# Optimization experiments

Hardware: AMD Instinct MI355X
Metric: run time of the kernel (lower is better)

## Reference

```python
import jax, jax.numpy as jnp
import numpy as np

D = 256      # input_dim
H = 8        # n_heads
HD = D // H  # head_dim = 32
S = 255      # num variables
S1 = S + 1   # new_seq (CLS + vars)
B = 4


def setup_inputs() -> dict:
    key = jax.random.key(0)
    ks = jax.random.split(key, 16)
    g = lambda k, shp, s=0.05: (jax.random.normal(k, shp, dtype=jnp.float32) * s)
    inp = {
        'desc_embeddings': jax.random.normal(ks[0], (B, S, D), dtype=jnp.float32),
        'name_value_embeddings': jax.random.normal(ks[1], (B, S1, D), dtype=jnp.float32),
        # q/k/v projections (nn.Linear: y = x @ W.T + b)
        'qW': g(ks[2], (D, D)), 'qb': jnp.zeros((D,), jnp.float32),
        'kW': g(ks[3], (D, D)), 'kb': jnp.zeros((D,), jnp.float32),
        'vW': g(ks[4], (D, D)), 'vb': jnp.zeros((D,), jnp.float32),
        # edge_update MLP: Linear(2D->D), LayerNorm(D), ReLU, Linear(D->D)
        'eW1': g(ks[5], (D, 2 * D)), 'eb1': jnp.zeros((D,), jnp.float32),
        'ln_g': jnp.ones((D,), jnp.float32), 'ln_b': jnp.zeros((D,), jnp.float32),
        'eW2': g(ks[6], (D, D)), 'eb2': jnp.zeros((D,), jnp.float32),
        # attn_proj: Linear(3*head_dim -> 1)
        'aW': g(ks[7], (1, 3 * HD)), 'ab': jnp.zeros((1,), jnp.float32),
    }
    return inp


def reference(desc_embeddings, name_value_embeddings, qW, qb, kW, kb, vW, vb,
              eW1, eb1, ln_g, ln_b, eW2, eb2, aW, ab):
    nve, desc = name_value_embeddings, desc_embeddings
    b, s1, _ = nve.shape
    s = s1 - 1

    # structure mask: CLS->Var on, Var->CLS off, Var-Var fully connected (self loops kept)
    new_adj = jnp.zeros((b, s1, s1), jnp.float32)
    new_adj = new_adj.at[:, 1:, 1:].set(1.0)
    new_adj = new_adj.at[:, 0, 1:].set(1.0)

    def lin(x, W, bb):
        return x @ W.T + bb

    q = lin(nve, qW, qb).reshape(b, s1, H, HD).transpose(0, 2, 1, 3)  # [B,H,S1,HD]
    k = lin(nve, kW, kb).reshape(b, s1, H, HD).transpose(0, 2, 1, 3)
    v = lin(nve, vW, vb).reshape(b, s1, H, HD).transpose(0, 2, 1, 3)

    # pairwise edge attributes [B,S1,S1,2D]
    di = jnp.broadcast_to(desc[:, :, None, :], (b, s, s, D))
    dj = jnp.broadcast_to(desc[:, None, :, :], (b, s, s, D))
    var_edge = jnp.concatenate([di, dj], axis=-1)              # [B,S,S,2D]
    cls_edge = jnp.concatenate([desc, desc], axis=-1)          # [B,S,2D]
    ea = jnp.zeros((b, s1, s1, 2 * D), jnp.float32)
    ea = ea.at[:, 1:, 1:].set(var_edge)
    ea = ea.at[:, 0, 1:].set(cls_edge)
    ea = ea.at[:, 1:, 0].set(cls_edge)

    # edge_update MLP (edge_type == 'mlp')
    h = lin(ea, eW1, eb1)
    mu = jnp.mean(h, axis=-1, keepdims=True)
    var = jnp.var(h, axis=-1, keepdims=True)
    h = ln_g * (h - mu) / jnp.sqrt(var + 1e-5) + ln_b
    h = jax.nn.relu(h)
    e = lin(h, eW2, eb2)                                       # [B,S1,S1,D]
    e = e.reshape(b, s1, s1, H, HD).transpose(0, 3, 1, 2, 4)    # [B,H,S1,S1,HD]
    e = e * new_adj[:, None, :, :, None]

    # attn_proj(cat(q_i, k_j, e_ij)) == q_i.wq + k_j.wk + e_ij.we + bias (gat_v1, no nonlinearity)
    wq, wk, we = aW[0, :HD], aW[0, HD:2 * HD], aW[0, 2 * HD:]
    logits = (jnp.einsum('bhid,d->bhi', q, wq)[:, :, :, None]
              + jnp.einsum('bhjd,d->bhj', k, wk)[:, :, None, :]
              + jnp.einsum('bhijd,d->bhij', e, we) + ab[0])    # [B,H,S1,S1]

    logits = logits + (new_adj[:, None] == 0).astype(logits.dtype) * -1e9
    attn = jax.nn.softmax(logits, axis=-1)                      # dropout omitted (eval)
    ctx = jnp.einsum('bhij,bhjd->bhid', attn, v)
    basis_outputs = ctx.transpose(0, 2, 1, 3)                   # [B,S1,H,HD]
    return basis_outputs, attn
```

## Files before the change

kernel.cpp:

```cpp
#include <hip/hip_runtime.h>
#include <math.h>

#define S 255
#define B 4

typedef _Float16 half8 __attribute__((ext_vector_type(8)));
typedef float f32x4 __attribute__((ext_vector_type(4)));

#define WS_APJ   0
#define WS_BPJ   131072
#define WS_VTF   262144
#define WS_ATT   393216
#define WS_AP    1441792
#define WS_GJ    1703936
#define WS_MFG   1966080
#define WS_CONST 1968128
#define WS_QLOG  1968192
#define WS_KLOG  1976384
#define WS_SA    1984576
#define WS_QA    1985600
#define WS_SB    1986624
#define WS_QB    1987648

__global__ __launch_bounds__(256) void k1(
    const float* __restrict__ desc, const float* __restrict__ nve,
    const float* __restrict__ qW, const float* __restrict__ qb,
    const float* __restrict__ kW, const float* __restrict__ kb,
    const float* __restrict__ vW, const float* __restrict__ vb,
    const float* __restrict__ eW1, const float* __restrict__ eb1,
    const float* __restrict__ eW2, const float* __restrict__ eb2,
    const float* __restrict__ aW, float* __restrict__ ws)
{
    const int blk = blockIdx.x;
    const int tid = threadIdx.x;
    __shared__ _Float16 Af[4096];
    __shared__ _Float16 Bf[4096];
    const int wave = tid >> 6, lane = tid & 63;
    const int m16 = lane & 15, quad = lane >> 4;
    const int sr = tid & 63, sko = (tid >> 6) * 16;
    const half8 z8 = {(_Float16)0,(_Float16)0,(_Float16)0,(_Float16)0,
                      (_Float16)0,(_Float16)0,(_Float16)0,(_Float16)0};

    if (blk < 192) {
        const float *X, *W; int M, wst, wof, jobt, sub = blk;
        if (sub < 64)       { X=nve;  W=vW;  M=1024; wst=256; wof=0;   jobt=0; }
        else if (sub < 128) { X=desc; W=eW1; M=1020; wst=512; wof=0;   jobt=1; sub-=64; }
        else                { X=desc; W=eW1; M=1020; wst=512; wof=256; jobt=2; sub-=128; }
        int mBase = (sub>>2)*64, nBase = (sub&3)*64;
        f32x4 acc[2][2] = {};
        for (int k0 = 0; k0 < 256; k0 += 64) {
            half8 xa[2], wb[2];
            int xr = mBase + sr, wr = nBase + sr;
            #pragma unroll
            for (int hh = 0; hh < 2; hh++) {
                int kk = k0 + sko + hh*8;
                if (xr < M) {
                    float4 x0 = *(const float4*)&X[xr*256 + kk];
                    float4 x1 = *(const float4*)&X[xr*256 + kk + 4];
                    half8 hv;
                    hv[0]=(_Float16)x0.x; hv[1]=(_Float16)x0.y; hv[2]=(_Float16)x0.z; hv[3]=(_Float16)x0.w;
                    hv[4]=(_Float16)x1.x; hv[5]=(_Float16)x1.y; hv[6]=(_Float16)x1.z; hv[7]=(_Float16)x1.w;
                    xa[hh] = hv;
                } else xa[hh] = z8;
                float4 w0 = *(const float4*)&W[wr*wst + wof + kk];
                float4 w1 = *(const float4*)&W[wr*wst + wof + kk + 4];
                half8 hw;
                hw[0]=(_Float16)w0.x; hw[1]=(_Float16)w0.y; hw[2]=(_Float16)w0.z; hw[3]=(_Float16)w0.w;
                hw[4]=(_Float16)w1.x; hw[5]=(_Float16)w1.y; hw[6]=(_Float16)w1.z; hw[7]=(_Float16)w1.w;
                wb[hh] = hw;
            }
            __syncthreads();
            #pragma unroll
            for (int hh = 0; hh < 2; hh++) {
                int krel = sko + hh*8;
                int c = krel >> 5, q2 = (krel >> 3) & 3;
                int ld = (sr & 15) + 16*q2, rt = sr >> 4;
                *(half8*)&Af[((rt*2 + c)*64 + ld)*8] = xa[hh];
                *(half8*)&Bf[((rt*2 + c)*64 + ld)*8] = wb[hh];
            }
            __syncthreads();
            int rt0 = (wave >> 1)*2, ct0 = (wave & 1)*2;
            #pragma unroll
            for (int c = 0; c < 2; c++) {
                half8 A0 = *(const half8*)&Af[(((rt0    )*2 + c)*64 + lane)*8];
                half8 A1 = *(const half8*)&Af[(((rt0 + 1)*2 + c)*64 + lane)*8];
                half8 B0 = *(const half8*)&Bf[(((ct0    )*2 + c)*64 + lane)*8];
                half8 B1 = *(const half8*)&Bf[(((ct0 + 1)*2 + c)*64 + lane)*8];
                acc[0][0] = __builtin_amdgcn_mfma_f32_16x16x32_f16(A0, B0, acc[0][0], 0,0,0);
                acc[0][1] = __builtin_amdgcn_mfma_f32_16x16x32_f16(A0, B1, acc[0][1], 0,0,0);
                acc[1][0] = __builtin_amdgcn_mfma_f32_16x16x32_f16(A1, B0, acc[1][0], 0,0,0);
                acc[1][1] = __builtin_amdgcn_mfma_f32_16x16x32_f16(A1, B1, acc[1][1], 0,0,0);
            }
        }
        int rt0 = (wave >> 1)*2, ct0 = (wave & 1)*2;
        if (jobt == 0) {
            _Float16* vtf = (_Float16*)(ws + WS_VTF);
            #pragma unroll
            for (int ci = 0; ci < 2; ci++) {
                int col = nBase + (ct0 + ci)*16 + m16;
                float bv = vb[col];
                int ct = col >> 4, n = col & 15;
                #pragma unroll
                for (int ri = 0; ri < 2; ri++)
                    #pragma unroll
                    for (int r = 0; r < 4; r++) {
                        int rr = mBase + (rt0 + ri)*16 + quad*4 + r;
                        int bb = rr >> 8, j = rr & 255;
                        int js = j >> 5, qv = (j >> 3) & 3, ev = j & 7;
                        float o = acc[ri][ci][r] + bv;
                        vtf[bb*65536 + (((ct*8 + js)*64 + n + 16*qv) << 3) + ev] = (_Float16)o;
                    }
            }
        } else {
            _Float16* OJ = (_Float16*)(ws + ((jobt == 1) ? WS_APJ : WS_BPJ));
            float* Sp = ws + ((jobt == 1) ? WS_SA : WS_SB);
            float* Qp = ws + ((jobt == 1) ? WS_QA : WS_QB);
            float svr[2][4] = {}, qvr[2][4] = {};
            #pragma unroll
            for (int ci = 0; ci < 2; ci++) {
                int col = nBase + (ct0 + ci)*16 + m16;
                float bv = (jobt == 1) ? eb1[col] : 0.f;
                int ks = col >> 5, q = (col >> 3) & 3, e = col & 7;
                #pragma unroll
                for (int ri = 0; ri < 2; ri++)
                    #pragma unroll
                    for (int r = 0; r < 4; r++) {
                        int rr = mBase + (rt0 + ri)*16 + quad*4 + r;
                        if (rr < 1020) {
                            float o = acc[ri][ci][r] + bv;
                            int bb = rr / 255;
                            int j = rr - bb*255 + 1;
                            int jt = j >> 4, mm = j & 15;
                            OJ[bb*65536 + (((jt*8 + ks)*64 + mm + 16*q) << 3) + e] = (_Float16)o;
                            if (jobt == 1) ws[WS_AP + rr*256 + col] = o;
                            svr[ri][r] += o;
                            qvr[ri][r] = fmaf(o, o, qvr[ri][r]);
                        }
                    }
            }
            #pragma unroll
            for (int ri = 0; ri < 2; ri++)
                #pragma unroll
                for (int r = 0; r < 4; r++) {
                    float s = svr[ri][r], q = qvr[ri][r];
                    #pragma unroll
                    for (int d = 1; d < 16; d <<= 1) {
                        s += __shfl_xor(s, d, 64);
                        q += __shfl_xor(q, d, 64);
                    }
                    int rr = mBase + (rt0 + ri)*16 + quad*4 + r;
                    if (m16 == 0 && rr < 1020) {
                        int bb = rr / 255;
                        int j = rr - bb*255 + 1;
                        atomicAdd(&Sp[bb*256 + j], s);
                        atomicAdd(&Qp[bb*256 + j], q);
                    }
                }
        }
    } else if (blk < 208) {
        {
            int d = tid;
            float f[16] = {0,0,0,0,0,0,0,0,0,0,0,0,0,0,0,0};
            for (int hd = 0; hd < 32; hd++) {
                float wq = aW[hd], wk = aW[32+hd];
                #pragma unroll
                for (int h = 0; h < 8; h++) {
                    f[h]   = fmaf(wq, qW[(h*32+hd)*256 + d], f[h]);
                    f[8+h] = fmaf(wk, kW[(h*32+hd)*256 + d], f[8+h]);
                }
            }
            int ksd = d >> 5, q2 = (d >> 3) & 3, jj = d & 7;
            #pragma unroll
            for (int n = 0; n < 16; n++)
                Bf[((ksd*64 + n + 16*q2))*8 + jj] = (_Float16)f[n];
        }
        __syncthreads();
        int mBase = (blk - 192)*64;
        f32x4 acc = {0.f,0.f,0.f,0.f};
        for (int k0 = 0; k0 < 256; k0 += 64) {
            half8 xa[2];
            #pragma unroll
            for (int hh = 0; hh < 2; hh++) {
                int kk = k0 + sko + hh*8;
                float4 x0 = *(const float4*)&nve[(mBase + sr)*256 + kk];
                float4 x1 = *(const float4*)&nve[(mBase + sr)*256 + kk + 4];
                half8 hv;
                hv[0]=(_Float16)x0.x; hv[1]=(_Float16)x0.y; hv[2]=(_Float16)x0.z; hv[3]=(_Float16)x0.w;
                hv[4]=(_Float16)x1.x; hv[5]=(_Float16)x1.y; hv[6]=(_Float16)x1.z; hv[7]=(_Float16)x1.w;
                xa[hh] = hv;
            }
            __syncthreads();
            #pragma unroll
            for (int hh = 0; hh < 2; hh++) {
                int krel = sko + hh*8;
                int c = krel >> 5, q2 = (krel >> 3) & 3;
                int ld = (sr & 15) + 16*q2, rt = sr >> 4;
                *(half8*)&Af[((rt*2 + c)*64 + ld)*8] = xa[hh];
            }
            __syncthreads();
            #pragma unroll
            for (int c = 0; c < 2; c++) {
                half8 A  = *(const half8*)&Af[((wave*2 + c)*64 + lane)*8];
                half8 Bv = *(const half8*)&Bf[(((k0 >> 5) + c)*64 + lane)*8];
                acc = __builtin_amdgcn_mfma_f32_16x16x32_f16(A, Bv, acc, 0,0,0);
            }
        }
        #pragma unroll
        for (int r = 0; r < 4; r++) {
            int rr = mBase + wave*16 + quad*4 + r;
            int bb = rr >> 8, tt2 = rr & 255;
            if (m16 < 8) ws[WS_QLOG + (bb*8 + m16)*256 + tt2] = acc[r];
            else         ws[WS_KLOG + (bb*8 + m16 - 8)*256 + tt2] = acc[r];
        }
    } else {
        _Float16* mfg = (_Float16*)(ws + WS_MFG);
        int k = tid;
        float a8[8] = {0,0,0,0,0,0,0,0};
        for (int hd = 0; hd < 32; hd++) {
            float we = aW[64+hd];
            #pragma unroll
            for (int h = 0; h < 8; h++)
                a8[h] = fmaf(we, eW2[(h*32+hd)*256 + k], a8[h]);
        }
        int ksd = k >> 5, q2 = (k >> 3) & 3, jj = k & 7;
        #pragma unroll
        for (int h = 0; h < 8; h++)
            mfg[((ksd*64 + h + 16*q2))*8 + jj] = (_Float16)a8[h];
        #pragma unroll
        for (int n = 8; n < 16; n++)
            mfg[((ksd*64 + n + 16*q2))*8 + jj] = (_Float16)0.f;
        {
            _Float16* apj = (_Float16*)(ws + WS_APJ);
            _Float16* bpj = (_Float16*)(ws + WS_BPJ);
            int ks0 = tid >> 5, qz = (tid >> 3) & 3, ez = tid & 7;
            int ad = ((ks0*64 + 16*qz) << 3) + ez;
            #pragma unroll
            for (int bb = 0; bb < 4; bb++) {
                apj[bb*65536 + ad] = (_Float16)0.f;
                bpj[bb*65536 + ad] = (_Float16)0.f;
            }
        }
        if (tid == 0) {
            #pragma unroll
            for (int h = 0; h < 8; h++) {
                float c = 0.f;
                for (int hd = 0; hd < 32; hd++) {
                    c = fmaf(aW[64+hd], eb2[h*32+hd], c);
                    c = fmaf(aW[hd],    qb [h*32+hd], c);
                    c = fmaf(aW[32+hd], kb [h*32+hd], c);
                }
                ws[WS_CONST + h] = c;
            }
        }
    }
}

__global__ __launch_bounds__(256) void k2(float* __restrict__ ws)
{
    int b = blockIdx.y;
    int x = blockIdx.x;
    int tid = threadIdx.x;
    int wave = tid >> 6, lane = tid & 63;
    int m16 = lane & 15, quad = lane >> 4;
    int rt = (x >> 2)*4 + (wave >> 1)*2;
    int ct = (x & 3)*4 + (wave & 1)*2;
    const _Float16* apj = (const _Float16*)(ws + WS_APJ) + b*65536;
    const _Float16* bpj = (const _Float16*)(ws + WS_BPJ) + b*65536;
    f32x4 acc[2][2] = {};
    #pragma unroll
    for (int ks = 0; ks < 8; ks++) {
        half8 A0 = *(const half8*)&apj[(((rt    )*8 + ks)*64 + lane) << 3];
        half8 A1 = *(const half8*)&apj[(((rt + 1)*8 + ks)*64 + lane) << 3];
        half8 B0 = *(const half8*)&bpj[(((ct    )*8 + ks)*64 + lane) << 3];
        half8 B1 = *(const half8*)&bpj[(((ct + 1)*8 + ks)*64 + lane) << 3];
        acc[0][0] = __builtin_amdgcn_mfma_f32_16x16x32_f16(A0, B0, acc[0][0], 0,0,0);
        acc[0][1] = __builtin_amdgcn_mfma_f32_16x16x32_f16(A0, B1, acc[0][1], 0,0,0);
        acc[1][0] = __builtin_amdgcn_mfma_f32_16x16x32_f16(A1, B0, acc[1][0], 0,0,0);
        acc[1][1] = __builtin_amdgcn_mfma_f32_16x16x32_f16(A1, B1, acc[1][1], 0,0,0);
    }
    float* gj = ws + WS_GJ + (size_t)b*65536;
    #pragma unroll
    for (int ci = 0; ci < 2; ci++) {
        int col = (ct + ci)*16 + m16;
        #pragma unroll
        for (int ri = 0; ri < 2; ri++)
            #pragma unroll
            for (int r = 0; r < 4; r++)
                gj[((rt + ri)*16 + quad*4 + r)*256 + col] = acc[ri][ci][r];
    }
}

__global__ __launch_bounds__(256, 4) void k3(
    const float* __restrict__ ln_g, const float* __restrict__ ln_b,
    const float* __restrict__ ab, const float* __restrict__ ws,
    float* __restrict__ out)
{
    int b = blockIdx.y, i = blockIdx.x;
    int tid = threadIdx.x;
    __shared__ float klds[2048];
    __shared__ float PL[2048];
    __shared__ float gL[256], bL[256], aL[256];
    __shared__ float2 st[256];
    __shared__ float baseh[8], mxs[8], sms[8];

    #pragma unroll
    for (int t = 0; t < 8; t++)
        klds[tid + t*256] = ws[WS_KLOG + b*2048 + tid + t*256];
    gL[tid] = ln_g[tid];
    bL[tid] = ln_b[tid];
    aL[tid] = (i >= 1) ? ws[WS_AP + ((size_t)(b*S + i - 1))*256 + tid] : 0.f;
    if (tid < 8)
        baseh[tid] = ws[WS_QLOG + (b*8+tid)*256 + i] + ab[0] + ws[WS_CONST + tid];
    {
        int j = tid;
        float2 v; v.x = 0.f; v.y = 0.f;
        if (j >= 1) {
            float sa, qa, sb, qb2, g;
            if (i >= 1) {
                sa = ws[WS_SA + b*256 + i]; qa = ws[WS_QA + b*256 + i];
                sb = ws[WS_SB + b*256 + j]; qb2 = ws[WS_QB + b*256 + j];
                g  = ws[WS_GJ + (size_t)b*65536 + i*256 + j];
            } else {
                sa = ws[WS_SA + b*256 + j]; qa = ws[WS_QA + b*256 + j];
                sb = ws[WS_SB + b*256 + j]; qb2 = ws[WS_QB + b*256 + j];
                g  = ws[WS_GJ + (size_t)b*65536 + j*256 + j];
            }
            float mu  = (sa + sb) * (1.0f/256.0f);
            float var = (qa + qb2 + 2.f*g) * (1.0f/256.0f) - mu*mu;
            float inv = rsqrtf(var + 1e-5f);
            v.x = inv; v.y = -mu*inv;
        }
        st[j] = v;
    }
    __syncthreads();

    int wave = tid >> 6, lane = tid & 63;
    int m16 = lane & 15, quad = lane >> 4;
    const _Float16* mfg = (const _Float16*)(ws + WS_MFG);
    const _Float16* bpj = (const _Float16*)(ws + WS_BPJ) + b*65536;
    const _Float16* apj = (const _Float16*)(ws + WS_APJ) + b*65536;
    f32x4 acc[4] = {};
    float2 sv[4];
    #pragma unroll
    for (int tt = 0; tt < 4; tt++)
        sv[tt] = st[(wave*4 + tt)*16 + m16];

    if (i >= 1) {
        #pragma unroll
        for (int ks = 0; ks < 8; ks++) {
            int k = ks*32 + quad*8;
            float4 a0 = *(const float4*)&aL[k], a1 = *(const float4*)&aL[k+4];
            float4 g0 = *(const float4*)&gL[k], g1 = *(const float4*)&gL[k+4];
            float4 b0 = *(const float4*)&bL[k], b1 = *(const float4*)&bL[k+4];
            half8 bf = *(const half8*)&mfg[(ks*64 + lane) << 3];
            float aa[8] = {a0.x,a0.y,a0.z,a0.w,a1.x,a1.y,a1.z,a1.w};
            float ga[8] = {g0.x,g0.y,g0.z,g0.w,g1.x,g1.y,g1.z,g1.w};
            float be[8] = {b0.x,b0.y,b0.z,b0.w,b1.x,b1.y,b1.z,b1.w};
            #pragma unroll
            for (int tt = 0; tt < 4; tt++) {
                half8 bp = *(const half8*)&bpj[(((wave*4 + tt)*8 + ks)*64 + lane) << 3];
                half8 af;
                #pragma unroll
                for (int e = 0; e < 8; e++) {
                    float c = (float)bp[e] + aa[e];
                    float w = fmaf(fmaf(c, sv[tt].x, sv[tt].y), ga[e], be[e]);
                    af[e] = (_Float16)fmaxf(w, 0.f);
                }
                acc[tt] = __builtin_amdgcn_mfma_f32_16x16x32_f16(af, bf, acc[tt], 0,0,0);
            }
        }
    } else {
        #pragma unroll
        for (int ks = 0; ks < 8; ks++) {
            int k = ks*32 + quad*8;
            float4 g0 = *(const float4*)&gL[k], g1 = *(const float4*)&gL[k+4];
            float4 b0 = *(const float4*)&bL[k], b1 = *(const float4*)&bL[k+4];
            half8 bf = *(const half8*)&mfg[(ks*64 + lane) << 3];
            float ga[8] = {g0.x,g0.y,g0.z,g0.w,g1.x,g1.y,g1.z,g1.w};
            float be[8] = {b0.x,b0.y,b0.z,b0.w,b1.x,b1.y,b1.z,b1.w};
            #pragma unroll
            for (int tt = 0; tt < 4; tt++) {
                int idx = ((((wave*4 + tt)*8 + ks)*64 + lane) << 3);
                half8 bp = *(const half8*)&bpj[idx];
                half8 ap = *(const half8*)&apj[idx];
                half8 af;
                #pragma unroll
                for (int e = 0; e < 8; e++) {
                    float c = (float)ap[e] + (float)bp[e];
                    float w = fmaf(fmaf(c, sv[tt].x, sv[tt].y), ga[e], be[e]);
                    af[e] = (_Float16)fmaxf(w, 0.f);
                }
                acc[tt] = __builtin_amdgcn_mfma_f32_16x16x32_f16(af, bf, acc[tt], 0,0,0);
            }
        }
    }

    if (m16 < 8) {
        float basev = baseh[m16];
        #pragma unroll
        for (int tt = 0; tt < 4; tt++)
            #pragma unroll
            for (int r = 0; r < 4; r++) {
                int jr = (wave*4 + tt)*16 + quad*4 + r;
                float val = basev + klds[m16*256 + jr];
                val += (jr == 0) ? -1e9f : acc[tt][r];
                PL[m16*256 + jr] = val;
            }
    }
    __syncthreads();

    {
        int h = tid >> 5, sg = tid & 31;
        float mv = -INFINITY;
        #pragma unroll
        for (int r = 0; r < 8; r++) mv = fmaxf(mv, PL[h*256 + sg + r*32]);
        #pragma unroll
        for (int off = 16; off >= 1; off >>= 1)
            mv = fmaxf(mv, __shfl_xor(mv, off, 64));
        if (sg == 0) mxs[h] = mv;
    }
    __syncthreads();
    float p[8];
    #pragma unroll
    for (int h = 0; h < 8; h++) p[h] = expf(PL[h*256 + tid] - mxs[h]);
    __syncthreads();
    #pragma unroll
    for (int h = 0; h < 8; h++) PL[h*256 + tid] = p[h];
    __syncthreads();
    {
        int h = tid >> 5, sg = tid & 31;
        float sv2 = 0.f;
        #pragma unroll
        for (int r = 0; r < 8; r++) sv2 += PL[h*256 + sg + r*32];
        #pragma unroll
        for (int off = 16; off >= 1; off >>= 1)
            sv2 += __shfl_xor(sv2, off, 64);
        if (sg == 0) sms[h] = sv2;
    }
    __syncthreads();

    float* attnOut = out + 262144;
    _Float16* att = (_Float16*)(ws + WS_ATT);
    int it = i >> 4, mi = i & 15;
    int js = tid >> 5, qj = (tid >> 3) & 3, ej = tid & 7;
    int fad = (((it*8 + js)*64 + mi + 16*qj) << 3) + ej;
    #pragma unroll
    for (int h = 0; h < 8; h++) {
        float a = p[h] / sms[h];
        attnOut[((b*8+h)*256 + i)*256 + tid] = a;
        att[(b*8+h)*65536 + fad] = (_Float16)a;
    }
}

__global__ __launch_bounds__(256) void k4(const float* __restrict__ ws,
                                          float* __restrict__ out)
{
    int blk = blockIdx.x;
    int b = blk >> 5, h = (blk >> 2) & 7, mq = blk & 3;
    int tid = threadIdx.x;
    int wave = tid >> 6, lane = tid & 63;
    int m16 = lane & 15, quad = lane >> 4;
    int it = mq*4 + wave;
    const _Float16* att = (const _Float16*)(ws + WS_ATT) + (size_t)(b*8 + h)*65536;
    const _Float16* vtf = (const _Float16*)(ws + WS_VTF) + (size_t)b*65536;
    int ct0 = h*2;
    f32x4 acc[2] = {};
    #pragma unroll
    for (int js = 0; js < 8; js++) {
        half8 A  = *(const half8*)&att[((it*8 + js)*64 + lane) << 3];
        half8 B0 = *(const half8*)&vtf[(((ct0    )*8 + js)*64 + lane) << 3];
        half8 B1 = *(const half8*)&vtf[(((ct0 + 1)*8 + js)*64 + lane) << 3];
        acc[0] = __builtin_amdgcn_mfma_f32_16x16x32_f16(A, B0, acc[0], 0,0,0);
        acc[1] = __builtin_amdgcn_mfma_f32_16x16x32_f16(A, B1, acc[1], 0,0,0);
    }
    #pragma unroll
    for (int nt = 0; nt < 2; nt++) {
        int col = h*32 + nt*16 + m16;
        #pragma unroll
        for (int r = 0; r < 4; r++) {
            int row = it*16 + quad*4 + r;
            out[(b*256 + row)*256 + col] = acc[nt][r];
        }
    }
}

extern "C" void kernel_launch(void* const* d_in, const int* in_sizes, int n_in,
                              void* d_out, int out_size, void* d_ws, size_t ws_size,
                              hipStream_t stream)
{
    const float* desc = (const float*)d_in[0];
    const float* nve  = (const float*)d_in[1];
    const float* qW   = (const float*)d_in[2];
    const float* qb   = (const float*)d_in[3];
    const float* kW   = (const float*)d_in[4];
    const float* kb   = (const float*)d_in[5];
    const float* vW   = (const float*)d_in[6];
    const float* vb   = (const float*)d_in[7];
    const float* eW1  = (const float*)d_in[8];
    const float* eb1  = (const float*)d_in[9];
    const float* ln_g = (const float*)d_in[10];
    const float* ln_b = (const float*)d_in[11];
    const float* eW2  = (const float*)d_in[12];
    const float* eb2  = (const float*)d_in[13];
    const float* aW   = (const float*)d_in[14];
    const float* ab   = (const float*)d_in[15];
    float* ws  = (float*)d_ws;
    float* out = (float*)d_out;

    hipMemsetAsync((char*)d_ws + (size_t)WS_SA*4, 0, 4096*4, stream);
    k1<<<dim3(209), 256, 0, stream>>>(desc, nve, qW, qb, kW, kb, vW, vb,
                                      eW1, eb1, eW2, eb2, aW, ws);
    k2<<<dim3(16, 4), 256, 0, stream>>>(ws);
    k3<<<dim3(256, 4), 256, 0, stream>>>(ln_g, ln_b, ab, ws, out);
    k4<<<dim3(128), 256, 0, stream>>>(ws, out);
}
```

Baseline: 137.3 us.

## Fuse LayerNorm statistics and attention-V product into k3, drop k2, k4 and memset

Removes the separate Gram-matrix kernel k2, the attention×V kernel k4, the workspace memset and the atomic row-sum/sum-of-squares accumulation from k1. Each k3 block now computes its own row statistics with MFMA tricks (ones vectors, self-products) and applies softmax(P)·V in-block from shared memory, normalising by the row sum at the end. The softmax scratch buffer is padded to a 272-float row stride to reduce LDS bank conflicts. This saves three launches and the global round-trips for the Gram matrix and the fp16 attention matrix, at the cost of redundant per-block MFMA work in k3 and some precision risk from fp16 conversions.

```diff
diff --git a/kernel.cpp b/kernel.cpp
--- a/kernel.cpp
+++ b/kernel.cpp
@@ -10,17 +10,18 @@
 #define WS_APJ   0
 #define WS_BPJ   131072
 #define WS_VTF   262144
-#define WS_ATT   393216
-#define WS_AP    1441792
-#define WS_GJ    1703936
-#define WS_MFG   1966080
-#define WS_CONST 1968128
-#define WS_QLOG  1968192
-#define WS_KLOG  1976384
-#define WS_SA    1984576
-#define WS_QA    1985600
-#define WS_SB    1986624
-#define WS_QB    1987648
+#define WS_AP    393216
+#define WS_MFG   654336
+#define WS_CONST 656384
+#define WS_QLOG  656392
+#define WS_KLOG  664584
+
+__device__ __forceinline__ half8 cvt8(float4 a, float4 b) {
+    half8 h;
+    h[0]=(_Float16)a.x; h[1]=(_Float16)a.y; h[2]=(_Float16)a.z; h[3]=(_Float16)a.w;
+    h[4]=(_Float16)b.x; h[5]=(_Float16)b.y; h[6]=(_Float16)b.z; h[7]=(_Float16)b.w;
+    return h;
+}
 
 __global__ __launch_bounds__(256) void k1(
     const float* __restrict__ desc, const float* __restrict__ nve,
@@ -54,20 +55,11 @@
             #pragma unroll
             for (int hh = 0; hh < 2; hh++) {
                 int kk = k0 + sko + hh*8;
-                if (xr < M) {
-                    float4 x0 = *(const float4*)&X[xr*256 + kk];
-                    float4 x1 = *(const float4*)&X[xr*256 + kk + 4];
-                    half8 hv;
-                    hv[0]=(_Float16)x0.x; hv[1]=(_Float16)x0.y; hv[2]=(_Float16)x0.z; hv[3]=(_Float16)x0.w;
-                    hv[4]=(_Float16)x1.x; hv[5]=(_Float16)x1.y; hv[6]=(_Float16)x1.z; hv[7]=(_Float16)x1.w;
-                    xa[hh] = hv;
-                } else xa[hh] = z8;
-                float4 w0 = *(const float4*)&W[wr*wst + wof + kk];
-                float4 w1 = *(const float4*)&W[wr*wst + wof + kk + 4];
-                half8 hw;
-                hw[0]=(_Float16)w0.x; hw[1]=(_Float16)w0.y; hw[2]=(_Float16)w0.z; hw[3]=(_Float16)w0.w;
-                hw[4]=(_Float16)w1.x; hw[5]=(_Float16)w1.y; hw[6]=(_Float16)w1.z; hw[7]=(_Float16)w1.w;
-                wb[hh] = hw;
+                if (xr < M) xa[hh] = cvt8(*(const float4*)&X[xr*256 + kk],
+                                          *(const float4*)&X[xr*256 + kk + 4]);
+                else xa[hh] = z8;
+                wb[hh] = cvt8(*(const float4*)&W[wr*wst + wof + kk],
+                              *(const float4*)&W[wr*wst + wof + kk + 4]);
             }
             __syncthreads();
             #pragma unroll
@@ -113,9 +105,6 @@
             }
         } else {
             _Float16* OJ = (_Float16*)(ws + ((jobt == 1) ? WS_APJ : WS_BPJ));
-            float* Sp = ws + ((jobt == 1) ? WS_SA : WS_SB);
-            float* Qp = ws + ((jobt == 1) ? WS_QA : WS_QB);
-            float svr[2][4] = {}, qvr[2][4] = {};
             #pragma unroll
             for (int ci = 0; ci < 2; ci++) {
                 int col = nBase + (ct0 + ci)*16 + m16;
@@ -133,29 +122,9 @@
                             int jt = j >> 4, mm = j & 15;
                             OJ[bb*65536 + (((jt*8 + ks)*64 + mm + 16*q) << 3) + e] = (_Float16)o;
                             if (jobt == 1) ws[WS_AP + rr*256 + col] = o;
-                            svr[ri][r] += o;
-                            qvr[ri][r] = fmaf(o, o, qvr[ri][r]);
                         }
                     }
             }
-            #pragma unroll
-            for (int ri = 0; ri < 2; ri++)
-                #pragma unroll
-                for (int r = 0; r < 4; r++) {
-                    float s = svr[ri][r], q = qvr[ri][r];
-                    #pragma unroll
-                    for (int d = 1; d < 16; d <<= 1) {
-                        s += __shfl_xor(s, d, 64);
-                        q += __shfl_xor(q, d, 64);
-                    }
-                    int rr = mBase + (rt0 + ri)*16 + quad*4 + r;
-                    if (m16 == 0 && rr < 1020) {
-                        int bb = rr / 255;
-                        int j = rr - bb*255 + 1;
-                        atomicAdd(&Sp[bb*256 + j], s);
-                        atomicAdd(&Qp[bb*256 + j], q);
-                    }
-                }
         }
     } else if (blk < 208) {
         {
@@ -182,12 +151,8 @@
             #pragma unroll
             for (int hh = 0; hh < 2; hh++) {
                 int kk = k0 + sko + hh*8;
-                float4 x0 = *(const float4*)&nve[(mBase + sr)*256 + kk];
-                float4 x1 = *(const float4*)&nve[(mBase + sr)*256 + kk + 4];
-                half8 hv;
-                hv[0]=(_Float16)x0.x; hv[1]=(_Float16)x0.y; hv[2]=(_Float16)x0.z; hv[3]=(_Float16)x0.w;
-                hv[4]=(_Float16)x1.x; hv[5]=(_Float16)x1.y; hv[6]=(_Float16)x1.z; hv[7]=(_Float16)x1.w;
-                xa[hh] = hv;
+                xa[hh] = cvt8(*(const float4*)&nve[(mBase + sr)*256 + kk],
+                              *(const float4*)&nve[(mBase + sr)*256 + kk + 4]);
             }
             __syncthreads();
             #pragma unroll
@@ -255,40 +220,7 @@
     }
 }
 
-__global__ __launch_bounds__(256) void k2(float* __restrict__ ws)
-{
-    int b = blockIdx.y;
-    int x = blockIdx.x;
-    int tid = threadIdx.x;
-    int wave = tid >> 6, lane = tid & 63;
-    int m16 = lane & 15, quad = lane >> 4;
-    int rt = (x >> 2)*4 + (wave >> 1)*2;
-    int ct = (x & 3)*4 + (wave & 1)*2;
-    const _Float16* apj = (const _Float16*)(ws + WS_APJ) + b*65536;
-    const _Float16* bpj = (const _Float16*)(ws + WS_BPJ) + b*65536;
-    f32x4 acc[2][2] = {};
-    #pragma unroll
-    for (int ks = 0; ks < 8; ks++) {
-        half8 A0 = *(const half8*)&apj[(((rt    )*8 + ks)*64 + lane) << 3];
-        half8 A1 = *(const half8*)&apj[(((rt + 1)*8 + ks)*64 + lane) << 3];
-        half8 B0 = *(const half8*)&bpj[(((ct    )*8 + ks)*64 + lane) << 3];
-        half8 B1 = *(const half8*)&bpj[(((ct + 1)*8 + ks)*64 + lane) << 3];
-        acc[0][0] = __builtin_amdgcn_mfma_f32_16x16x32_f16(A0, B0, acc[0][0], 0,0,0);
-        acc[0][1] = __builtin_amdgcn_mfma_f32_16x16x32_f16(A0, B1, acc[0][1], 0,0,0);
-        acc[1][0] = __builtin_amdgcn_mfma_f32_16x16x32_f16(A1, B0, acc[1][0], 0,0,0);
-        acc[1][1] = __builtin_amdgcn_mfma_f32_16x16x32_f16(A1, B1, acc[1][1], 0,0,0);
-    }
-    float* gj = ws + WS_GJ + (size_t)b*65536;
-    #pragma unroll
-    for (int ci = 0; ci < 2; ci++) {
-        int col = (ct + ci)*16 + m16;
-        #pragma unroll
-        for (int ri = 0; ri < 2; ri++)
-            #pragma unroll
-            for (int r = 0; r < 4; r++)
-                gj[((rt + ri)*16 + quad*4 + r)*256 + col] = acc[ri][ci][r];
-    }
-}
+#define PLS 272
 
 __global__ __launch_bounds__(256, 4) void k3(
     const float* __restrict__ ln_g, const float* __restrict__ ln_b,
@@ -298,33 +230,105 @@
     int b = blockIdx.y, i = blockIdx.x;
     int tid = threadIdx.x;
     __shared__ float klds[2048];
-    __shared__ float PL[2048];
+    __shared__ float PL[8*PLS];
     __shared__ float gL[256], bL[256], aL[256];
     __shared__ float2 st[256];
-    __shared__ float baseh[8], mxs[8], sms[8];
+    __shared__ float stG[256], stSB[256], stQB[256], stSA[256], stQA[256];
+    __shared__ float baseh[8], mxs[8], sms[8], saqa[8];
+
+    int wave = tid >> 6, lane = tid & 63;
+    int m16 = lane & 15, quad = lane >> 4;
+    const half8 z8 = {(_Float16)0,(_Float16)0,(_Float16)0,(_Float16)0,
+                      (_Float16)0,(_Float16)0,(_Float16)0,(_Float16)0};
+    half8 ones8;
+    #pragma unroll
+    for (int e = 0; e < 8; e++) ones8[e] = (_Float16)1.0f;
 
     #pragma unroll
     for (int t = 0; t < 8; t++)
         klds[tid + t*256] = ws[WS_KLOG + b*2048 + tid + t*256];
     gL[tid] = ln_g[tid];
     bL[tid] = ln_b[tid];
-    aL[tid] = (i >= 1) ? ws[WS_AP + ((size_t)(b*S + i - 1))*256 + tid] : 0.f;
+    float av = (i >= 1) ? ws[WS_AP + ((size_t)(b*S + i - 1))*256 + tid] : 0.f;
+    aL[tid] = av;
+    {
+        float s1 = av, s2 = av*av;
+        #pragma unroll
+        for (int off = 32; off >= 1; off >>= 1) {
+            s1 += __shfl_xor(s1, off, 64);
+            s2 += __shfl_xor(s2, off, 64);
+        }
+        if (lane == 0) { saqa[wave] = s1; saqa[4+wave] = s2; }
+    }
     if (tid < 8)
         baseh[tid] = ws[WS_QLOG + (b*8+tid)*256 + i] + ab[0] + ws[WS_CONST + tid];
+    __syncthreads();
+
+    const _Float16* mfg = (const _Float16*)(ws + WS_MFG);
+    const _Float16* bpj = (const _Float16*)(ws + WS_BPJ) + b*65536;
+    const _Float16* apj = (const _Float16*)(ws + WS_APJ) + b*65536;
+    const _Float16* vtf = (const _Float16*)(ws + WS_VTF) + b*65536;
+
+    if (i >= 1) {
+        #pragma unroll
+        for (int tl4 = 0; tl4 < 4; tl4++) {
+            int tl = wave*4 + tl4;
+            f32x4 accGS = {}, accQB = {};
+            #pragma unroll
+            for (int ks = 0; ks < 8; ks++) {
+                half8 bb = *(const half8*)&bpj[((tl*8+ks)*64 + lane) << 3];
+                half8 ags;
+                if (m16 == 0)
+                    ags = cvt8(*(const float4*)&aL[ks*32 + quad*8],
+                               *(const float4*)&aL[ks*32 + quad*8 + 4]);
+                else if (m16 == 1) ags = ones8;
+                else ags = z8;
+                accGS = __builtin_amdgcn_mfma_f32_16x16x32_f16(ags, bb, accGS, 0,0,0);
+                accQB = __builtin_amdgcn_mfma_f32_16x16x32_f16(bb,  bb, accQB, 0,0,0);
+            }
+            int j = tl*16 + m16;
+            if (quad == 0) { stG[j] = accGS[0]; stSB[j] = accGS[1]; }
+            if (quad == (m16 >> 2)) stQB[j] = accQB[m16 & 3];
+        }
+    } else {
+        #pragma unroll
+        for (int tl4 = 0; tl4 < 4; tl4++) {
+            int tl = wave*4 + tl4;
+            f32x4 accSB = {}, accSA = {}, accG = {}, accQA = {}, accQB = {};
+            #pragma unroll
+            for (int ks = 0; ks < 8; ks++) {
+                int idx = ((tl*8+ks)*64 + lane) << 3;
+                half8 bb = *(const half8*)&bpj[idx];
+                half8 aa = *(const half8*)&apj[idx];
+                half8 a1 = (m16 == 0) ? ones8 : z8;
+                accSB = __builtin_amdgcn_mfma_f32_16x16x32_f16(a1, bb, accSB, 0,0,0);
+                accSA = __builtin_amdgcn_mfma_f32_16x16x32_f16(a1, aa, accSA, 0,0,0);
+                accG  = __builtin_amdgcn_mfma_f32_16x16x32_f16(aa, bb, accG,  0,0,0);
+                accQA = __builtin_amdgcn_mfma_f32_16x16x32_f16(aa, aa, accQA, 0,0,0);
+                accQB = __builtin_amdgcn_mfma_f32_16x16x32_f16(bb, bb, accQB, 0,0,0);
+            }
+            int j = tl*16 + m16;
+            if (quad == 0) { stSB[j] = accSB[0]; stSA[j] = accSA[0]; }
+            if (quad == (m16 >> 2)) {
+                int r = m16 & 3;
+                stG[j] = accG[r]; stQA[j] = accQA[r]; stQB[j] = accQB[r];
+            }
+        }
+    }
+    __syncthreads();
+
     {
         int j = tid;
         float2 v; v.x = 0.f; v.y = 0.f;
         if (j >= 1) {
-            float sa, qa, sb, qb2, g;
+            float sa, qa;
             if (i >= 1) {
-                sa = ws[WS_SA + b*256 + i]; qa = ws[WS_QA + b*256 + i];
-                sb = ws[WS_SB + b*256 + j]; qb2 = ws[WS_QB + b*256 + j];
-                g  = ws[WS_GJ + (size_t)b*65536 + i*256 + j];
+                sa = saqa[0] + saqa[1] + saqa[2] + saqa[3];
+                qa = saqa[4] + saqa[5] + saqa[6] + saqa[7];
             } else {
-                sa = ws[WS_SA + b*256 + j]; qa = ws[WS_QA + b*256 + j];
-                sb = ws[WS_SB + b*256 + j]; qb2 = ws[WS_QB + b*256 + j];
-                g  = ws[WS_GJ + (size_t)b*65536 + j*256 + j];
-            }
+                sa = stSA[j]; qa = stQA[j];
+            }
+            float sb = stSB[j], qb2 = stQB[j], g = stG[j];
             float mu  = (sa + sb) * (1.0f/256.0f);
             float var = (qa + qb2 + 2.f*g) * (1.0f/256.0f) - mu*mu;
             float inv = rsqrtf(var + 1e-5f);
@@ -334,11 +338,6 @@
     }
     __syncthreads();
 
-    int wave = tid >> 6, lane = tid & 63;
-    int m16 = lane & 15, quad = lane >> 4;
-    const _Float16* mfg = (const _Float16*)(ws + WS_MFG);
-    const _Float16* bpj = (const _Float16*)(ws + WS_BPJ) + b*65536;
-    const _Float16* apj = (const _Float16*)(ws + WS_APJ) + b*65536;
     f32x4 acc[4] = {};
     float2 sv[4];
     #pragma unroll
@@ -404,7 +403,7 @@
                 int jr = (wave*4 + tt)*16 + quad*4 + r;
                 float val = basev + klds[m16*256 + jr];
                 val += (jr == 0) ? -1e9f : acc[tt][r];
-                PL[m16*256 + jr] = val;
+                PL[m16*PLS + jr] = val;
             }
     }
     __syncthreads();
@@ -413,7 +412,7 @@
         int h = tid >> 5, sg = tid & 31;
         float mv = -INFINITY;
         #pragma unroll
-        for (int r = 0; r < 8; r++) mv = fmaxf(mv, PL[h*256 + sg + r*32]);
+        for (int r = 0; r < 8; r++) mv = fmaxf(mv, PL[h*PLS + sg + r*32]);
         #pragma unroll
         for (int off = 16; off >= 1; off >>= 1)
             mv = fmaxf(mv, __shfl_xor(mv, off, 64));
@@ -422,16 +421,16 @@
     __syncthreads();
     float p[8];
     #pragma unroll
-    for (int h = 0; h < 8; h++) p[h] = expf(PL[h*256 + tid] - mxs[h]);
+    for (int h = 0; h < 8; h++) p[h] = expf(PL[h*PLS + tid] - mxs[h]);
     __syncthreads();
     #pragma unroll
-    for (int h = 0; h < 8; h++) PL[h*256 + tid] = p[h];
+    for (int h = 0; h < 8; h++) PL[h*PLS + tid] = p[h];
     __syncthreads();
     {
         int h = tid >> 5, sg = tid & 31;
         float sv2 = 0.f;
         #pragma unroll
-        for (int r = 0; r < 8; r++) sv2 += PL[h*256 + sg + r*32];
+        for (int r = 0; r < 8; r++) sv2 += PL[h*PLS + sg + r*32];
         #pragma unroll
         for (int off = 16; off >= 1; off >>= 1)
             sv2 += __shfl_xor(sv2, off, 64);
@@ -440,46 +439,35 @@
     __syncthreads();
 
     float* attnOut = out + 262144;
-    _Float16* att = (_Float16*)(ws + WS_ATT);
-    int it = i >> 4, mi = i & 15;
-    int js = tid >> 5, qj = (tid >> 3) & 3, ej = tid & 7;
-    int fad = (((it*8 + js)*64 + mi + 16*qj) << 3) + ej;
     #pragma unroll
-    for (int h = 0; h < 8; h++) {
-        float a = p[h] / sms[h];
-        attnOut[((b*8+h)*256 + i)*256 + tid] = a;
-        att[(b*8+h)*65536 + fad] = (_Float16)a;
-    }
-}
-
-__global__ __launch_bounds__(256) void k4(const float* __restrict__ ws,
-                                          float* __restrict__ out)
-{
-    int blk = blockIdx.x;
-    int b = blk >> 5, h = (blk >> 2) & 7, mq = blk & 3;
-    int tid = threadIdx.x;
-    int wave = tid >> 6, lane = tid & 63;
-    int m16 = lane & 15, quad = lane >> 4;
-    int it = mq*4 + wave;
-    const _Float16* att = (const _Float16*)(ws + WS_ATT) + (size_t)(b*8 + h)*65536;
-    const _Float16* vtf = (const _Float16*)(ws + WS_VTF) + (size_t)b*65536;
-    int ct0 = h*2;
-    f32x4 acc[2] = {};
-    #pragma unroll
-    for (int js = 0; js < 8; js++) {
-        half8 A  = *(const half8*)&att[((it*8 + js)*64 + lane) << 3];
-        half8 B0 = *(const half8*)&vtf[(((ct0    )*8 + js)*64 + lane) << 3];
-        half8 B1 = *(const half8*)&vtf[(((ct0 + 1)*8 + js)*64 + lane) << 3];
-        acc[0] = __builtin_amdgcn_mfma_f32_16x16x32_f16(A, B0, acc[0], 0,0,0);
-        acc[1] = __builtin_amdgcn_mfma_f32_16x16x32_f16(A, B1, acc[1], 0,0,0);
-    }
-    #pragma unroll
-    for (int nt = 0; nt < 2; nt++) {
-        int col = h*32 + nt*16 + m16;
-        #pragma unroll
-        for (int r = 0; r < 4; r++) {
-            int row = it*16 + quad*4 + r;
-            out[(b*256 + row)*256 + col] = acc[nt][r];
+    for (int h = 0; h < 8; h++)
+        attnOut[((b*8+h)*256 + i)*256 + tid] = p[h] / sms[h];
+
+    {
+        f32x4 cacc[4] = {};
+        int ct0 = wave*4;
+        #pragma unroll
+        for (int js = 0; js < 8; js++) {
+            half8 af;
+            if (m16 < 8) {
+                float4 p0 = *(const float4*)&PL[m16*PLS + js*32 + quad*8];
+                float4 p1 = *(const float4*)&PL[m16*PLS + js*32 + quad*8 + 4];
+                af = cvt8(p0, p1);
+            } else af = z8;
+            #pragma unroll
+            for (int cl = 0; cl < 4; cl++) {
+                half8 bf = *(const half8*)&vtf[(((ct0+cl)*8 + js)*64 + lane) << 3];
+                cacc[cl] = __builtin_amdgcn_mfma_f32_16x16x32_f16(af, bf, cacc[cl], 0,0,0);
+            }
+        }
+        #pragma unroll
+        for (int cl = 0; cl < 4; cl++) {
+            int ct = ct0 + cl;
+            int h = ct >> 1;
+            if (quad == (h >> 2)) {
+                float rs = 1.0f / sms[h];
+                out[(b*256 + i)*256 + ct*16 + m16] = cacc[cl][h & 3] * rs;
+            }
         }
     }
 }
@@ -507,10 +495,7 @@
     float* ws  = (float*)d_ws;
     float* out = (float*)d_out;
 
-    hipMemsetAsync((char*)d_ws + (size_t)WS_SA*4, 0, 4096*4, stream);
     k1<<<dim3(209), 256, 0, stream>>>(desc, nve, qW, qb, kW, kb, vW, vb,
                                       eW1, eb1, eW2, eb2, aW, ws);
-    k2<<<dim3(16, 4), 256, 0, stream>>>(ws);
     k3<<<dim3(256, 4), 256, 0, stream>>>(ln_g, ln_b, ab, ws, out);
-    k4<<<dim3(128), 256, 0, stream>>>(ws, out);
 }
```

Result: no change. 137.1 us (-0.1%).
